# Kernel optimization log

Hardware: AMD Instinct MI355X
Metric: run time of the kernel (lower is better)

## Reference

```python
import jax, jax.numpy as jnp
import numpy as np

N_NODES = 100000
N_EDGES = 1600000
D_FEAT = 50
ALPHA = 0.1


def setup_inputs() -> dict:
    key = jax.random.key(0)
    k1, k2, k3, k4, k5 = jax.random.split(key, 5)
    x = jax.random.normal(k1, (N_NODES, D_FEAT), dtype=jnp.float32)
    h = jax.random.normal(k2, (N_NODES, D_FEAT), dtype=jnp.float32)
    adj_vals = jax.random.uniform(k3, (N_EDGES,), dtype=jnp.float32)
    adj_rows = jax.random.randint(k4, (N_EDGES,), 0, N_NODES, dtype=jnp.int32)
    adj_cols = jax.random.randint(k5, (N_EDGES,), 0, N_NODES, dtype=jnp.int32)
    return {"x": x, "h": h, "adj_vals": adj_vals,
            "adj_rows": adj_rows, "adj_cols": adj_cols}


def reference(x, h, adj_vals, adj_rows, adj_cols):
    # SpMM: out[r] += vals[e] * x[cols[e]] for edges e with rows[e] == r.
    # Equivalent to the original per-column torch.sparse.mm loop, fused.
    msgs = adj_vals[:, None] * x[adj_cols]          # [E, d] gather + scale
    ax = jax.ops.segment_sum(msgs, adj_rows, num_segments=N_NODES)  # [N, d]
    return (1.0 - ALPHA) * ax + ALPHA * h
```

## Files before the change

kernel.cpp:

```cpp
#include <hip/hip_runtime.h>
#include <hip/hip_bf16.h>

#define N_NODES 100000
#define N_EDGES 1600000
#define D_FEAT 50
#define ALPHA 0.1f

#define BINSHIFT 7
#define BINROWS 128
#define NBINS ((N_NODES + BINROWS - 1) / BINROWS)
#define SCK 5120
#define NSCB ((N_EDGES + SCK - 1) / SCK)
#define SORT_CAP 2560
#define XB_STRIDE 64
#define SCAN_ITEMS ((NBINS + 63) / 64)

__global__ void init_out_kernel(const float* __restrict__ h,
                                float* __restrict__ out, int n) {
    int idx = blockIdx.x * blockDim.x + threadIdx.x;
    if (idx < n) out[idx] = ALPHA * h[idx];
}

__global__ void scatter_atomic_kernel(const float* __restrict__ x,
                                      const float* __restrict__ vals,
                                      const int* __restrict__ rows,
                                      const int* __restrict__ cols,
                                      float* __restrict__ out) {
    long long idx = (long long)blockIdx.x * blockDim.x + threadIdx.x;
    long long total = (long long)N_EDGES * D_FEAT;
    if (idx >= total) return;
    int e = (int)(idx / D_FEAT);
    int d = (int)(idx % D_FEAT);
    float contrib = (1.0f - ALPHA) * vals[e] * x[(long long)cols[e] * D_FEAT + d];
    atomicAdd(&out[(long long)rows[e] * D_FEAT + d], contrib);
}


__global__ __launch_bounds__(256) void cvt_x_kernel(const float* __restrict__ x,
                                                    ushort* __restrict__ xb) {
    int i = blockIdx.x * 256 + threadIdx.x;
    if (i >= N_NODES * XB_STRIDE) return;
    int r = i >> 6, d = i & (XB_STRIDE - 1);
    float v = (d < D_FEAT) ? x[r * D_FEAT + d] : 0.0f;
    unsigned u = __float_as_uint(v);
    unsigned rnd = (u + 0x7FFFu + ((u >> 16) & 1u)) >> 16;
    xb[i] = (ushort)rnd;
}

__global__ __launch_bounds__(256) void hist_bins_kernel(
        const int* __restrict__ rows, int* __restrict__ bin_count) {
    __shared__ int lh[NBINS];
    for (int i = threadIdx.x; i < NBINS; i += 256) lh[i] = 0;
    __syncthreads();
    int tid = blockIdx.x * 256 + threadIdx.x;
    int nthreads = gridDim.x * 256;
    const int E4 = N_EDGES / 4;
    for (int i = tid; i < E4; i += nthreads) {
        int4 r = ((const int4*)rows)[i];
        atomicAdd(&lh[r.x >> BINSHIFT], 1);
        atomicAdd(&lh[r.y >> BINSHIFT], 1);
        atomicAdd(&lh[r.z >> BINSHIFT], 1);
        atomicAdd(&lh[r.w >> BINSHIFT], 1);
    }
    __syncthreads();
    for (int i = threadIdx.x; i < NBINS; i += 256) {
        int c = lh[i];
        if (c) atomicAdd(&bin_count[i], c);
    }
}

__global__ void scan_bins_kernel(const int* __restrict__ bin_count,
                                 int* __restrict__ bin_start,
                                 int* __restrict__ bin_cursor) {
    int lane = threadIdx.x;
    int base = lane * SCAN_ITEMS;
    int loc[SCAN_ITEMS];
    int s = 0;
    #pragma unroll
    for (int i = 0; i < SCAN_ITEMS; ++i) {
        int idx = base + i;
        int c = (idx < NBINS) ? bin_count[idx] : 0;
        loc[i] = s;
        s += c;
    }
    int incl = s;
    #pragma unroll
    for (int off = 1; off < 64; off <<= 1) {
        int u = __shfl_up(incl, off);
        if (lane >= off) incl += u;
    }
    int excl = incl - s;
    #pragma unroll
    for (int i = 0; i < SCAN_ITEMS; ++i) {
        int idx = base + i;
        if (idx < NBINS) {
            int ex = excl + loc[i];
            bin_start[idx] = ex;
            bin_cursor[idx] = ex;
        }
    }
    if (lane == 0) bin_start[NBINS] = N_EDGES;
}

__global__ __launch_bounds__(1024) void bin_scatter_kernel(
        const float* __restrict__ vals,
        const int* __restrict__ rows,
        const int* __restrict__ cols,
        int* __restrict__ bin_cursor,
        float2* __restrict__ packed) {
    __shared__ float2 sbuf[SCK];
    __shared__ ushort sbin[SCK];
    __shared__ int lh[NBINS];
    __shared__ int lws[NBINS];
    __shared__ int gbase[NBINS];
    int t = threadIdx.x;
    int cs = blockIdx.x * SCK;
    int ce = cs + SCK;
    if (ce > N_EDGES) ce = N_EDGES;
    int cn = ce - cs;
    for (int i = t; i < NBINS; i += 1024) lh[i] = 0;
    __syncthreads();
    float2 pp[5]; int bb[5]; int k = 0;
    for (int e = cs + t; e < ce; e += 1024) {
        int r = rows[e];
        int b = r >> BINSHIFT;
        float2 p;
        p.x = __int_as_float(((r & (BINROWS - 1)) << 17) | cols[e]);
        p.y = vals[e] * (1.0f - ALPHA);
        pp[k] = p; bb[k] = b; ++k;
        atomicAdd(&lh[b], 1);
    }
    __syncthreads();
    if (t < 64) {
        int base = t * SCAN_ITEMS;
        int loc[SCAN_ITEMS];
        int s2 = 0;
        #pragma unroll
        for (int i = 0; i < SCAN_ITEMS; ++i) {
            int idx = base + i;
            int c = (idx < NBINS) ? lh[idx] : 0;
            loc[i] = s2; s2 += c;
        }
        int incl = s2;
        #pragma unroll
        for (int off = 1; off < 64; off <<= 1) {
            int u = __shfl_up(incl, off);
            if (t >= off) incl += u;
        }
        int excl = incl - s2;
        #pragma unroll
        for (int i = 0; i < SCAN_ITEMS; ++i) {
            int idx = base + i;
            if (idx < NBINS) lws[idx] = excl + loc[i];
        }
    }
    __syncthreads();
    for (int i = t; i < NBINS; i += 1024) {
        int c = lh[i];
        gbase[i] = c ? atomicAdd(&bin_cursor[i], c) : 0;
        lh[i] = lws[i];
    }
    __syncthreads();
    for (int i = 0; i < k; ++i) {
        int pos = atomicAdd(&lh[bb[i]], 1);
        sbuf[pos] = pp[i];
        sbin[pos] = (ushort)bb[i];
    }
    __syncthreads();
    for (int j = t; j < cn; j += 1024) {
        int b = sbin[j];
        packed[gbase[b] + (j - lws[b])] = sbuf[j];
    }
}

__global__ __launch_bounds__(512) void spmm_fused_kernel(
        const ushort* __restrict__ xb,
        const float* __restrict__ h,
        const int* __restrict__ bin_start,
        const float2* __restrict__ packed,
        float* __restrict__ out) {
    __shared__ float2 srt[SORT_CAP];
    __shared__ int rstart[BINROWS];
    __shared__ int cur[BINROWS];
    __shared__ int cnt[BINROWS];
    int bin = blockIdx.x;
    int t = threadIdx.x;
    int s = bin_start[bin];
    int e = bin_start[bin + 1];
    int n = e - s;
    if (n > SORT_CAP) n = SORT_CAP;
    if (t < BINROWS) cnt[t] = 0;
    __syncthreads();
    float2 st[5]; int sr[5]; int k = 0;
    for (int i = t; i < n; i += 512) {
        float2 p = packed[s + i];
        int r = __float_as_int(p.x) >> 17;
        st[k] = p; sr[k] = r; ++k;
        atomicAdd(&cnt[r], 1);
    }
    __syncthreads();
    if (t < BINROWS) rstart[t] = cnt[t];
    __syncthreads();
    for (int off = 1; off < BINROWS; off <<= 1) {
        int u = 0;
        if (t < BINROWS && t >= off) u = rstart[t - off];
        __syncthreads();
        if (t < BINROWS) rstart[t] += u;
        __syncthreads();
    }
    if (t < BINROWS) {
        int ex = rstart[t] - cnt[t];
        rstart[t] = ex;
        cur[t] = ex;
    }
    __syncthreads();
    for (int i = 0; i < k; ++i) {
        int pos = atomicAdd(&cur[sr[i]], 1);
        float2 q;
        q.x = __int_as_float(__float_as_int(st[i].x) & 0x1FFFF);
        q.y = st[i].y;
        srt[pos] = q;
    }
    __syncthreads();
    int lane = t & 63;
    int wv = t >> 6;
    int half = lane >> 5;
    int fl = lane & 31;
    int r0 = bin << BINSHIFT;
    for (int r = wv; r < BINROWS; r += 8) {
        int gr = r0 + r;
        if (gr >= N_NODES) break;
        int es = rstart[r];
        int ee = cur[r];
        float a0 = 0.0f, a1 = 0.0f, b0 = 0.0f, b1 = 0.0f;
        int ei = es;
        for (; ei + 4 <= ee; ei += 4) {
            float2 p = srt[ei + half];
            float2 q = srt[ei + 2 + half];
            int cp = __float_as_int(p.x);
            int cq = __float_as_int(q.x);
            unsigned wp = *(const unsigned*)(xb + (cp << 6) + 2 * fl);
            unsigned wq = *(const unsigned*)(xb + (cq << 6) + 2 * fl);
            a0 += p.y * __uint_as_float(wp << 16);
            a1 += p.y * __uint_as_float(wp & 0xFFFF0000u);
            b0 += q.y * __uint_as_float(wq << 16);
            b1 += q.y * __uint_as_float(wq & 0xFFFF0000u);
        }
        for (; ei < ee; ei += 2) {
            int idx = ei + half;
            bool valid = idx < ee;
            float2 p = srt[valid ? idx : es];
            float v = valid ? p.y : 0.0f;
            int cp = __float_as_int(p.x);
            unsigned wp = *(const unsigned*)(xb + (cp << 6) + 2 * fl);
            a0 += v * __uint_as_float(wp << 16);
            a1 += v * __uint_as_float(wp & 0xFFFF0000u);
        }
        a0 += b0;
        a1 += b1;
        a0 += __shfl_xor(a0, 32);
        a1 += __shfl_xor(a1, 32);
        if (lane < D_FEAT / 2) {
            int o = gr * D_FEAT + 2 * fl;
            float2 hv = *(const float2*)(h + o);
            float2 rr;
            rr.x = a0 + ALPHA * hv.x;
            rr.y = a1 + ALPHA * hv.y;
            *(float2*)(out + o) = rr;
        }
    }
}

extern "C" void kernel_launch(void* const* d_in, const int* in_sizes, int n_in,
                              void* d_out, int out_size, void* d_ws, size_t ws_size,
                              hipStream_t stream) {
    const float* x        = (const float*)d_in[0];
    const float* h        = (const float*)d_in[1];
    const float* adj_vals = (const float*)d_in[2];
    const int*   adj_rows = (const int*)d_in[3];
    const int*   adj_cols = (const int*)d_in[4];
    float* out = (float*)d_out;

    size_t n_ints = (size_t)NBINS * 3 + 1;
    n_ints = (n_ints + 1) & ~(size_t)1;
    size_t needed = n_ints * 4 + (size_t)N_EDGES * 8
                  + (size_t)N_NODES * XB_STRIDE * 2;

    if (ws_size < needed) {
        int n_out = N_NODES * D_FEAT;
        init_out_kernel<<<(n_out + 255) / 256, 256, 0, stream>>>(h, out, n_out);
        long long total = (long long)N_EDGES * D_FEAT;
        scatter_atomic_kernel<<<(int)((total + 255) / 256), 256, 0, stream>>>(
            x, adj_vals, adj_rows, adj_cols, out);
        return;
    }

    int* bin_count  = (int*)d_ws;
    int* bin_start  = bin_count + NBINS;
    int* bin_cursor = bin_start + NBINS + 1;
    float2* packed  = (float2*)((int*)d_ws + n_ints);
    ushort* xb      = (ushort*)(packed + N_EDGES);

    hipMemsetAsync(bin_count, 0, (size_t)NBINS * 4, stream);
    cvt_x_kernel<<<(N_NODES * XB_STRIDE + 255) / 256, 256, 0, stream>>>(x, xb);
    hist_bins_kernel<<<256, 256, 0, stream>>>(adj_rows, bin_count);
    scan_bins_kernel<<<1, 64, 0, stream>>>(bin_count, bin_start, bin_cursor);
    bin_scatter_kernel<<<NSCB, 1024, 0, stream>>>(
        adj_vals, adj_rows, adj_cols, bin_cursor, packed);
    spmm_fused_kernel<<<NBINS, 512, 0, stream>>>(
        xb, h, bin_start, packed, out);
}
```

Measured before the change: 205.0 us.

## Halve bin size and re-read edges instead of caching in registers

```diff
diff --git a/kernel.cpp b/kernel.cpp
--- a/kernel.cpp
+++ b/kernel.cpp
@@ -6,12 +6,12 @@
 #define D_FEAT 50
 #define ALPHA 0.1f
 
-#define BINSHIFT 7
-#define BINROWS 128
+#define BINSHIFT 6
+#define BINROWS 64
 #define NBINS ((N_NODES + BINROWS - 1) / BINROWS)
 #define SCK 5120
 #define NSCB ((N_EDGES + SCK - 1) / SCK)
-#define SORT_CAP 2560
+#define SORT_CAP 1280
 #define XB_STRIDE 64
 #define SCAN_ITEMS ((NBINS + 63) / 64)
 
@@ -120,16 +120,8 @@
     int cn = ce - cs;
     for (int i = t; i < NBINS; i += 1024) lh[i] = 0;
     __syncthreads();
-    float2 pp[5]; int bb[5]; int k = 0;
-    for (int e = cs + t; e < ce; e += 1024) {
-        int r = rows[e];
-        int b = r >> BINSHIFT;
-        float2 p;
-        p.x = __int_as_float(((r & (BINROWS - 1)) << 17) | cols[e]);
-        p.y = vals[e] * (1.0f - ALPHA);
-        pp[k] = p; bb[k] = b; ++k;
-        atomicAdd(&lh[b], 1);
-    }
+    for (int e = cs + t; e < ce; e += 1024)
+        atomicAdd(&lh[rows[e] >> BINSHIFT], 1);
     __syncthreads();
     if (t < 64) {
         int base = t * SCAN_ITEMS;
@@ -161,10 +153,15 @@
         lh[i] = lws[i];
     }
     __syncthreads();
-    for (int i = 0; i < k; ++i) {
-        int pos = atomicAdd(&lh[bb[i]], 1);
-        sbuf[pos] = pp[i];
-        sbin[pos] = (ushort)bb[i];
+    for (int e = cs + t; e < ce; e += 1024) {
+        int r = rows[e];
+        int b = r >> BINSHIFT;
+        int pos = atomicAdd(&lh[b], 1);
+        float2 p;
+        p.x = __int_as_float(((r & (BINROWS - 1)) << 17) | cols[e]);
+        p.y = vals[e] * (1.0f - ALPHA);
+        sbuf[pos] = p;
+        sbin[pos] = (ushort)b;
     }
     __syncthreads();
     for (int j = t; j < cn; j += 1024) {
@@ -191,34 +188,28 @@
     if (n > SORT_CAP) n = SORT_CAP;
     if (t < BINROWS) cnt[t] = 0;
     __syncthreads();
-    float2 st[5]; int sr[5]; int k = 0;
+    for (int i = t; i < n; i += 512)
+        atomicAdd(&cnt[__float_as_int(packed[s + i].x) >> 17], 1);
+    __syncthreads();
+    if (t < 64) {
+        int c = cnt[t];
+        int incl = c;
+        #pragma unroll
+        for (int off = 1; off < 64; off <<= 1) {
+            int u = __shfl_up(incl, off);
+            if (t >= off) incl += u;
+        }
+        rstart[t] = incl - c;
+        cur[t] = incl - c;
+    }
+    __syncthreads();
     for (int i = t; i < n; i += 512) {
         float2 p = packed[s + i];
-        int r = __float_as_int(p.x) >> 17;
-        st[k] = p; sr[k] = r; ++k;
-        atomicAdd(&cnt[r], 1);
-    }
-    __syncthreads();
-    if (t < BINROWS) rstart[t] = cnt[t];
-    __syncthreads();
-    for (int off = 1; off < BINROWS; off <<= 1) {
-        int u = 0;
-        if (t < BINROWS && t >= off) u = rstart[t - off];
-        __syncthreads();
-        if (t < BINROWS) rstart[t] += u;
-        __syncthreads();
-    }
-    if (t < BINROWS) {
-        int ex = rstart[t] - cnt[t];
-        rstart[t] = ex;
-        cur[t] = ex;
-    }
-    __syncthreads();
-    for (int i = 0; i < k; ++i) {
-        int pos = atomicAdd(&cur[sr[i]], 1);
+        int pk = __float_as_int(p.x);
+        int pos = atomicAdd(&cur[pk >> 17], 1);
         float2 q;
-        q.x = __int_as_float(__float_as_int(st[i].x) & 0x1FFFF);
-        q.y = st[i].y;
+        q.x = __int_as_float(pk & 0x1FFFF);
+        q.y = p.y;
         srt[pos] = q;
     }
     __syncthreads();
@@ -231,7 +222,7 @@
         int gr = r0 + r;
         if (gr >= N_NODES) break;
         int es = rstart[r];
-        int ee = cur[r];
+        int ee = es + cnt[r];
         float a0 = 0.0f, a1 = 0.0f, b0 = 0.0f, b1 = 0.0f;
         int ei = es;
         for (; ei + 4 <= ee; ei += 4) {
```

Result: no change. 201.3 us (-1.8%).
